# Kernel optimization log

Measured on AMD Instinct MI355X. Metric: run time of the kernel, lower is better.

Reference implementation:

```python
import jax, jax.numpy as jnp
import numpy as np

N, D, K = 8192, 4096, 8
F_HID = D // 4  # 1024


def setup_inputs() -> dict:
    key = jax.random.key(0)
    ks = jax.random.split(key, 8)
    s1 = 1.0 / np.sqrt(2 * D)
    s2 = 1.0 / np.sqrt(F_HID)
    sr = 1.0 / np.sqrt(D)
    return {
        "h_anchor": jax.random.normal(ks[0], (N, D), jnp.float32),
        "h_mask": jax.random.normal(ks[1], (N, D), jnp.float32),
        "Wr": jax.random.normal(ks[2], (K, D), jnp.float32) * sr,
        "br": jnp.zeros((K,), jnp.float32),
        "W1": jax.random.normal(ks[3], (K, F_HID, 2 * D), jnp.float32) * s1,
        "b1": jnp.zeros((K, F_HID), jnp.float32),
        "W2": jax.random.normal(ks[4], (K, D, F_HID), jnp.float32) * s2,
        "b2": jnp.zeros((K, D), jnp.float32),
    }


def reference(h_anchor, h_mask, Wr, br, W1, b1, W2, b2):
    # routing weights: softmax(h_mask @ Wr^T + br) -> [N, K]
    weights = jax.nn.softmax(h_mask @ Wr.T + br, axis=-1)
    # conditioned input: [N, 2D]
    conditioned = jnp.concatenate([h_anchor, h_mask], axis=-1)
    # all-expert first GEMM: [K, N, F]
    h1 = jnp.einsum("nc,kfc->knf", conditioned, W1) + b1[:, None, :]
    h1 = jax.nn.gelu(h1, approximate=False)  # torch nn.GELU default = exact erf
    # second GEMM: [K, N, D]
    expert_out = jnp.einsum("knf,kdf->knd", h1, W2) + b2[:, None, :]
    # softmax-weighted combine over experts -> [N, D]
    return jnp.einsum("knd,nk->nd", expert_out, weights)
```

## Files before the change

### kernel.cpp

```cpp
#include <hip/hip_runtime.h>
#include <hip/hip_bf16.h>
#include <math.h>

typedef __bf16 bf16_t;
typedef __bf16 bf16x8 __attribute__((ext_vector_type(8)));
typedef float  f32x4  __attribute__((ext_vector_type(4)));

#define AS1 __attribute__((address_space(1)))
#define AS3 __attribute__((address_space(3)))

__device__ __forceinline__ void gload_lds16(const bf16_t* g, char* l) {
  __builtin_amdgcn_global_load_lds((const AS1 void*)g, (AS3 void*)l, 16, 0, 0);
}

static constexpr int N_ROWS = 8192;
static constexpr int DDIM   = 4096;
static constexpr int KEXP   = 8;
static constexpr int FHID   = 1024;
static constexpr int KD     = 8192;

__global__ __launch_bounds__(256)
void routing_kernel(const float* __restrict__ hm, const float* __restrict__ Wr,
                    const float* __restrict__ br, float* __restrict__ wgt) {
  const int n = blockIdx.x;
  const int t = threadIdx.x;
  const int wid = t >> 6;
  const float4* row = (const float4*)(hm + (size_t)n * DDIM);
  float4 x[4];
#pragma unroll
  for (int j = 0; j < 4; ++j) x[j] = row[t + j * 256];
  __shared__ float red[KEXP][4];
  float part[KEXP];
#pragma unroll
  for (int k = 0; k < KEXP; ++k) {
    const float4* wr = (const float4*)(Wr + (size_t)k * DDIM);
    float s = 0.f;
#pragma unroll
    for (int j = 0; j < 4; ++j) {
      float4 w4 = wr[t + j * 256];
      s += x[j].x * w4.x + x[j].y * w4.y + x[j].z * w4.z + x[j].w * w4.w;
    }
#pragma unroll
    for (int off = 32; off > 0; off >>= 1) s += __shfl_down(s, off);
    part[k] = s;
  }
  if ((t & 63) == 0) {
#pragma unroll
    for (int k = 0; k < KEXP; ++k) red[k][wid] = part[k];
  }
  __syncthreads();
  if (t == 0) {
    float lg[KEXP];
    float mx = -1e30f;
#pragma unroll
    for (int k = 0; k < KEXP; ++k) {
      lg[k] = red[k][0] + red[k][1] + red[k][2] + red[k][3] + br[k];
      mx = fmaxf(mx, lg[k]);
    }
    float sum = 0.f;
#pragma unroll
    for (int k = 0; k < KEXP; ++k) { lg[k] = expf(lg[k] - mx); sum += lg[k]; }
    float inv = 1.f / sum;
#pragma unroll
    for (int k = 0; k < KEXP; ++k) wgt[(size_t)n * KEXP + k] = lg[k] * inv;
  }
}

__device__ __forceinline__ bf16x8 cvt8(float4 f0, float4 f1) {
  bf16x8 o;
  o[0] = (bf16_t)f0.x; o[1] = (bf16_t)f0.y; o[2] = (bf16_t)f0.z; o[3] = (bf16_t)f0.w;
  o[4] = (bf16_t)f1.x; o[5] = (bf16_t)f1.y; o[6] = (bf16_t)f1.z; o[7] = (bf16_t)f1.w;
  return o;
}

__global__ __launch_bounds__(256)
void conv_cond_kernel(const float* __restrict__ ha, const float* __restrict__ hm,
                      bf16_t* __restrict__ A) {
  size_t c = (size_t)blockIdx.x * 256 + threadIdx.x;
  int n   = (int)(c >> 10);
  int pos = ((int)c & 1023) * 8;
  const float* src = (pos < DDIM) ? ha + (size_t)n * DDIM + pos
                                  : hm + (size_t)n * DDIM + (pos - DDIM);
  float4 f0 = ((const float4*)src)[0];
  float4 f1 = ((const float4*)src)[1];
  *(bf16x8*)(A + c * 8) = cvt8(f0, f1);
}

__global__ __launch_bounds__(256)
void conv_cast_kernel(const float* __restrict__ in, bf16_t* __restrict__ out) {
  size_t c = (size_t)blockIdx.x * 256 + threadIdx.x;
  float4 f0 = ((const float4*)(in + c * 8))[0];
  float4 f1 = ((const float4*)(in + c * 8))[1];
  *(bf16x8*)(out + c * 8) = cvt8(f0, f1);
}

__global__ __launch_bounds__(256)
void conv_w2_kernel(const float* __restrict__ W2, bf16_t* __restrict__ B2) {
  size_t c = (size_t)blockIdx.x * 256 + threadIdx.x;
  int f8 = (int)(c & 127);
  int d  = (int)((c >> 7) & 4095);
  int k  = (int)(c >> 19);
  const float* src = W2 + ((size_t)k * DDIM + d) * FHID + f8 * 8;
  float4 f0 = ((const float4*)src)[0];
  float4 f1 = ((const float4*)src)[1];
  *(bf16x8*)(B2 + (size_t)d * KD + k * FHID + f8 * 8) = cvt8(f0, f1);
}

template <int MODE, int NCOLS>
__global__ __launch_bounds__(512, 2)
void gemm256_kernel(const bf16_t* __restrict__ Amat, const bf16_t* __restrict__ Bmat,
                    void* __restrict__ Cout, const float* __restrict__ bias,
                    const float* __restrict__ wgt) {
  constexpr int BM = 256, BN = 256, BK = 64;
  constexpr int NKT = KD / BK;
  __shared__ char lds_raw[2 * 65536];

  const int tid  = threadIdx.x;
  const int wid  = tid >> 6;
  const int lane = tid & 63;
  const int wr   = wid >> 2;
  const int wc   = wid & 3;

  constexpr int NBN    = NCOLS / BN;
  constexpr int NWIN_N = NBN / 16;
  const int bid = blockIdx.x;
  const int w   = bid >> 8;
  const int sl  = bid & 255;
  const int xcd = sl & 7;
  const int cu  = sl >> 3;
  const int wm  = w / NWIN_N, wn = w % NWIN_N;
  const int bm  = wm * 16 + ((xcd >> 1) << 2) + (cu & 3);
  const int bn  = wn * 16 + ((xcd & 1) << 3) + (cu >> 2);
  const int arow0 = bm * BM;
  const int brow0 = bn * BN;

  const bf16_t* sA[2][2];
  const bf16_t* sB[2][2];
#pragma unroll
  for (int h = 0; h < 2; ++h)
#pragma unroll
    for (int i = 0; i < 2; ++i) {
      int p   = tid * 16 + i * 8192;
      int l   = p ^ (((p >> 7) & 3) << 4) ^ (((p >> 9) & 1) << 6);
      int row = l >> 7, c = l & 127;
      sA[h][i] = Amat + (size_t)(arow0 + h * 128 + row) * KD + (c >> 1);
      sB[h][i] = Bmat + (size_t)(brow0 + h * 128 + row) * KD + (c >> 1);
    }

  const int j = lane >> 4;
  int aoff0[8], boff0[4];
#pragma unroll
  for (int mi = 0; mi < 8; ++mi) {
    int row = wr * 128 + mi * 16 + (lane & 15);
    aoff0[mi] = row * 128 + ((j ^ (row & 3)) << 4) + (((row >> 2) & 1) << 6);
  }
#pragma unroll
  for (int ni = 0; ni < 4; ++ni) {
    int row = wc * 64 + ni * 16 + (lane & 15);
    boff0[ni] = 32768 + row * 128 + ((j ^ (row & 3)) << 4) + (((row >> 2) & 1) << 6);
  }

  f32x4 acc[8][4];
  f32x4 zero = {0.f, 0.f, 0.f, 0.f};
#pragma unroll
  for (int mi = 0; mi < 8; ++mi)
#pragma unroll
    for (int ni = 0; ni < 4; ++ni) acc[mi][ni] = zero;

#define STAGEA(H, TAU)                                                          \
  { const size_t ko = (size_t)((TAU) & (NKT - 1)) * BK;                         \
    char* db = lds_raw + (((TAU) & 1) * 65536) + (H) * 16384 + (wid << 10);     \
    gload_lds16(sA[H][0] + ko, db);                                             \
    gload_lds16(sA[H][1] + ko, db + 8192); }
#define STAGEB(H, TAU)                                                          \
  { const size_t ko = (size_t)((TAU) & (NKT - 1)) * BK;                         \
    char* db = lds_raw + (((TAU) & 1) * 65536) + 32768 + (H) * 16384 + (wid << 10); \
    gload_lds16(sB[H][0] + ko, db);                                             \
    gload_lds16(sB[H][1] + ko, db + 8192); }

  STAGEB(0, 0) STAGEA(0, 0) STAGEA(1, 0) STAGEB(1, 0) STAGEB(0, 1)
  asm volatile("s_waitcnt vmcnt(2)" ::: "memory");
  __builtin_amdgcn_s_barrier();
  __builtin_amdgcn_sched_barrier(0);

  bf16x8 bb[4];

#define SB __builtin_amdgcn_sched_barrier(0);
#define CLUSTER(MI, HH)                                                         \
    _Pragma("unroll")                                                           \
    for (int ni = 0; ni < 4; ++ni)                                              \
      acc[(HH) * 4 + (MI)][ni] = __builtin_amdgcn_mfma_f32_16x16x32_bf16(       \
          aq[MI], bb[ni], acc[(HH) * 4 + (MI)][ni], 0, 0, 0);

#define PHASE(BUFO, HH, SS, STG, GATE)                                          \
  {                                                                             \
    STG;                                                                        \
    SB                                                                          \
    bf16x8 aq[4];                                                               \
    aq[0] = *(const bf16x8*)(lds_raw + (BUFO) + (aoff0[(HH)*4+0] ^ ((SS)*64))); \
    SB                                                                          \
    if ((HH) == 0) {                                                            \
      _Pragma("unroll")                                                         \
      for (int ni = 0; ni < 4; ++ni)                                            \
        bb[ni] = *(const bf16x8*)(lds_raw + (BUFO) + (boff0[ni] ^ ((SS)*64)));  \
      SB                                                                        \
    }                                                                           \
    aq[1] = *(const bf16x8*)(lds_raw + (BUFO) + (aoff0[(HH)*4+1] ^ ((SS)*64))); \
    SB                                                                          \
    aq[2] = *(const bf16x8*)(lds_raw + (BUFO) + (aoff0[(HH)*4+2] ^ ((SS)*64))); \
    SB                                                                          \
    aq[3] = *(const bf16x8*)(lds_raw + (BUFO) + (aoff0[(HH)*4+3] ^ ((SS)*64))); \
    SB                                                                          \
    __builtin_amdgcn_s_setprio(1);                                              \
    asm volatile("s_waitcnt lgkmcnt(3)" ::: "memory");                          \
    SB                                                                          \
    CLUSTER(0, HH)                                                              \
    SB                                                                          \
    asm volatile("s_waitcnt lgkmcnt(2)" ::: "memory");                          \
    SB                                                                          \
    CLUSTER(1, HH)                                                              \
    SB                                                                          \
    asm volatile("s_waitcnt lgkmcnt(1)" ::: "memory");                          \
    SB                                                                          \
    CLUSTER(2, HH)                                                              \
    SB                                                                          \
    asm volatile("s_waitcnt lgkmcnt(0)" ::: "memory");                          \
    SB                                                                          \
    CLUSTER(3, HH)                                                              \
    SB                                                                          \
    __builtin_amdgcn_s_setprio(0);                                              \
    if (GATE) {                                                                 \
      asm volatile("s_waitcnt vmcnt(2)" ::: "memory");                          \
      SB                                                                        \
    }                                                                           \
    __builtin_amdgcn_s_barrier();                                               \
    SB                                                                          \
  }

  for (int t = 0; t < NKT; t += 2) {
    PHASE(0,     0, 0, STAGEA(0, t + 1), 0)
    PHASE(0,     1, 0, STAGEA(1, t + 1), 0)
    PHASE(0,     0, 1, STAGEB(1, t + 1), 0)
    PHASE(0,     1, 1, STAGEB(0, t + 2), 1)
    PHASE(65536, 0, 0, STAGEA(0, t + 2), 0)
    PHASE(65536, 1, 0, STAGEA(1, t + 2), 0)
    PHASE(65536, 0, 1, STAGEB(1, t + 2), 0)
    PHASE(65536, 1, 1, STAGEB(0, t + 3), 1)
  }
#undef PHASE
#undef CLUSTER
#undef SB
#undef STAGEA
#undef STAGEB

  const int grow0 = arow0 + wr * 128 + ((lane >> 4) << 2);
  const int gcol0 = brow0 + wc * 64 + (lane & 15);

  if constexpr (MODE == 1) {
    bf16_t* __restrict__ H = (bf16_t*)Cout;
    const int kexp = brow0 >> 10;
#pragma unroll
    for (int mi = 0; mi < 8; ++mi) {
      float wn4[4];
#pragma unroll
      for (int r = 0; r < 4; ++r)
        wn4[r] = wgt[(size_t)(grow0 + mi * 16 + r) * KEXP + kexp];
#pragma unroll
      for (int ni = 0; ni < 4; ++ni) {
        int col = gcol0 + ni * 16;
        float bv = bias[col];
#pragma unroll
        for (int r = 0; r < 4; ++r) {
          int n = grow0 + mi * 16 + r;
          float x = acc[mi][ni][r] + bv;
          float g = 0.5f * x * (1.f + erff(x * 0.70710678118654752f));
          H[(size_t)n * KD + col] = (bf16_t)(g * wn4[r]);
        }
      }
    }
  } else {
    float* __restrict__ O = (float*)Cout;
    float bcol[4][KEXP];
#pragma unroll
    for (int ni = 0; ni < 4; ++ni)
#pragma unroll
      for (int k = 0; k < KEXP; ++k)
        bcol[ni][k] = bias[(size_t)k * NCOLS + gcol0 + ni * 16];
#pragma unroll
    for (int mi = 0; mi < 8; ++mi)
#pragma unroll
      for (int r = 0; r < 4; ++r) {
        int n = grow0 + mi * 16 + r;
        const float4* wp = (const float4*)(wgt + (size_t)n * KEXP);
        float4 wa = wp[0], wb = wp[1];
        float w8[KEXP] = {wa.x, wa.y, wa.z, wa.w, wb.x, wb.y, wb.z, wb.w};
#pragma unroll
        for (int ni = 0; ni < 4; ++ni) {
          float bb2 = 0.f;
#pragma unroll
          for (int k = 0; k < KEXP; ++k) bb2 += w8[k] * bcol[ni][k];
          O[(size_t)n * NCOLS + gcol0 + ni * 16] = acc[mi][ni][r] + bb2;
        }
      }
  }
}

extern "C" void kernel_launch(void* const* d_in, const int* in_sizes, int n_in,
                              void* d_out, int out_size, void* d_ws, size_t ws_size,
                              hipStream_t stream) {
  const float* h_anchor = (const float*)d_in[0];
  const float* h_mask   = (const float*)d_in[1];
  const float* Wr       = (const float*)d_in[2];
  const float* br       = (const float*)d_in[3];
  const float* W1       = (const float*)d_in[4];
  const float* b1       = (const float*)d_in[5];
  const float* W2       = (const float*)d_in[6];
  const float* b2       = (const float*)d_in[7];
  float* out = (float*)d_out;

  char* ws = (char*)d_ws;
  bf16_t* Abf  = (bf16_t*)(ws);
  bf16_t* W1bf = (bf16_t*)(ws + ((size_t)128 << 20));
  bf16_t* W2bf = (bf16_t*)(ws + ((size_t)256 << 20));
  bf16_t* H1s  = (bf16_t*)(ws + ((size_t)320 << 20));
  float*  wgt  = (float*) (ws + ((size_t)448 << 20));

  routing_kernel<<<N_ROWS, 256, 0, stream>>>(h_mask, Wr, br, wgt);
  conv_cond_kernel<<<(N_ROWS * KD / 8) / 256, 256, 0, stream>>>(h_anchor, h_mask, Abf);
  conv_cast_kernel<<<(KEXP * FHID * 2 * DDIM / 8) / 256, 256, 0, stream>>>(W1, W1bf);
  conv_w2_kernel<<<(KEXP * DDIM * FHID / 8) / 256, 256, 0, stream>>>(W2, W2bf);

  gemm256_kernel<1, 8192><<<(N_ROWS / 256) * (KD / 256), 512, 0, stream>>>(
      Abf, W1bf, (void*)H1s, b1, wgt);
  gemm256_kernel<2, 4096><<<(N_ROWS / 256) * (DDIM / 256), 512, 0, stream>>>(
      H1s, W2bf, (void*)out, b2, wgt);
}
```

Baseline: 1.522 ms.

## Switch GEMM to 32x32x16 MFMA with pre-swizzled LDS layout and simpler pipeline

Rewrites the main GEMM inner loop to use 32x32x16 bf16 MFMA instructions instead of 16x16x32. Operand tiles are staged into LDS in a lane-contiguous layout, so each lane reads its fragment with a plain linear offset and no XOR swizzle. The K-loop now runs one 64-wide k-tile per iteration in four sub-phases, with only two barriers per tile instead of one per phase. The larger MFMA tile is meant to cut LDS reads per FLOP and issue overhead, and the fewer barriers reduce synchronisation cost. The risks are LDS bank conflicts from the new layout and a changed epilogue mapping that must match the 32x32 accumulator layout exactly.

```diff
diff --git a/kernel.cpp b/kernel.cpp
--- a/kernel.cpp
+++ b/kernel.cpp
@@ -5,6 +5,7 @@
 typedef __bf16 bf16_t;
 typedef __bf16 bf16x8 __attribute__((ext_vector_type(8)));
 typedef float  f32x4  __attribute__((ext_vector_type(4)));
+typedef float  f32x16 __attribute__((ext_vector_type(16)));
 
 #define AS1 __attribute__((address_space(1)))
 #define AS3 __attribute__((address_space(3)))
@@ -111,7 +112,7 @@
 void gemm256_kernel(const bf16_t* __restrict__ Amat, const bf16_t* __restrict__ Bmat,
                     void* __restrict__ Cout, const float* __restrict__ bias,
                     const float* __restrict__ wgt) {
-  constexpr int BM = 256, BN = 256, BK = 64;
+  constexpr int BK = 64;
   constexpr int NKT = KD / BK;
   __shared__ char lds_raw[2 * 65536];
 
@@ -121,7 +122,7 @@
   const int wr   = wid >> 2;
   const int wc   = wid & 3;
 
-  constexpr int NBN    = NCOLS / BN;
+  constexpr int NBN    = NCOLS / 256;
   constexpr int NWIN_N = NBN / 16;
   const int bid = blockIdx.x;
   const int w   = bid >> 8;
@@ -131,176 +132,154 @@
   const int wm  = w / NWIN_N, wn = w % NWIN_N;
   const int bm  = wm * 16 + ((xcd >> 1) << 2) + (cu & 3);
   const int bn  = wn * 16 + ((xcd & 1) << 3) + (cu >> 2);
-  const int arow0 = bm * BM;
-  const int brow0 = bn * BN;
-
-  const bf16_t* sA[2][2];
-  const bf16_t* sB[2][2];
-#pragma unroll
-  for (int h = 0; h < 2; ++h)
-#pragma unroll
-    for (int i = 0; i < 2; ++i) {
-      int p   = tid * 16 + i * 8192;
-      int l   = p ^ (((p >> 7) & 3) << 4) ^ (((p >> 9) & 1) << 6);
-      int row = l >> 7, c = l & 127;
-      sA[h][i] = Amat + (size_t)(arow0 + h * 128 + row) * KD + (c >> 1);
-      sB[h][i] = Bmat + (size_t)(brow0 + h * 128 + row) * KD + (c >> 1);
-    }
-
-  const int j = lane >> 4;
-  int aoff0[8], boff0[4];
-#pragma unroll
-  for (int mi = 0; mi < 8; ++mi) {
-    int row = wr * 128 + mi * 16 + (lane & 15);
-    aoff0[mi] = row * 128 + ((j ^ (row & 3)) << 4) + (((row >> 2) & 1) << 6);
-  }
-#pragma unroll
-  for (int ni = 0; ni < 4; ++ni) {
-    int row = wc * 64 + ni * 16 + (lane & 15);
-    boff0[ni] = 32768 + row * 128 + ((j ^ (row & 3)) << 4) + (((row >> 2) & 1) << 6);
-  }
-
-  f32x4 acc[8][4];
-  f32x4 zero = {0.f, 0.f, 0.f, 0.f};
-#pragma unroll
-  for (int mi = 0; mi < 8; ++mi)
-#pragma unroll
-    for (int ni = 0; ni < 4; ++ni) acc[mi][ni] = zero;
-
-#define STAGEA(H, TAU)                                                          \
-  { const size_t ko = (size_t)((TAU) & (NKT - 1)) * BK;                         \
-    char* db = lds_raw + (((TAU) & 1) * 65536) + (H) * 16384 + (wid << 10);     \
-    gload_lds16(sA[H][0] + ko, db);                                             \
-    gload_lds16(sA[H][1] + ko, db + 8192); }
-#define STAGEB(H, TAU)                                                          \
-  { const size_t ko = (size_t)((TAU) & (NKT - 1)) * BK;                         \
-    char* db = lds_raw + (((TAU) & 1) * 65536) + 32768 + (H) * 16384 + (wid << 10); \
-    gload_lds16(sB[H][0] + ko, db);                                             \
-    gload_lds16(sB[H][1] + ko, db + 8192); }
-
-  STAGEB(0, 0) STAGEA(0, 0) STAGEA(1, 0) STAGEB(1, 0) STAGEB(0, 1)
-  asm volatile("s_waitcnt vmcnt(2)" ::: "memory");
+  const int arow0 = bm * 256;
+  const int brow0 = bn * 256;
+
+  const int b0 = 2 * wid, b1 = 2 * wid + 1;
+  const int dA0 = ((b0 >> 2) & 1) * 16384 + (b0 >> 3) * 4096 + (b0 & 3) * 1024;
+  const int dA1 = ((b1 >> 2) & 1) * 16384 + (b1 >> 3) * 4096 + (b1 & 3) * 1024;
+  const int dB0 = 32768 + (b0 >> 3) * 8192 + (b0 & 7) * 1024;
+  const int dB1 = 32768 + (b1 >> 3) * 8192 + (b1 & 7) * 1024;
+  const bf16_t* srcA0 = Amat + (size_t)(arow0 + ((b0 >> 2) & 1) * 128 + (b0 & 3) * 32 + (lane & 31)) * KD
+                        + (b0 >> 3) * 16 + (lane >> 5) * 8;
+  const bf16_t* srcA1 = Amat + (size_t)(arow0 + ((b1 >> 2) & 1) * 128 + (b1 & 3) * 32 + (lane & 31)) * KD
+                        + (b1 >> 3) * 16 + (lane >> 5) * 8;
+  const bf16_t* srcB0 = Bmat + (size_t)(brow0 + (b0 & 7) * 32 + (lane & 31)) * KD
+                        + (b0 >> 3) * 16 + (lane >> 5) * 8;
+  const bf16_t* srcB1 = Bmat + (size_t)(brow0 + (b1 & 7) * 32 + (lane & 31)) * KD
+                        + (b1 >> 3) * 16 + (lane >> 5) * 8;
+
+  f32x16 acc[4][2];
+#pragma unroll
+  for (int mi = 0; mi < 4; ++mi)
+#pragma unroll
+    for (int nj = 0; nj < 2; ++nj)
+#pragma unroll
+      for (int r = 0; r < 16; ++r) acc[mi][nj][r] = 0.f;
+
+  gload_lds16(srcA0, lds_raw + dA0);
+  gload_lds16(srcA1, lds_raw + dA1);
+  gload_lds16(srcB0, lds_raw + dB0);
+  gload_lds16(srcB1, lds_raw + dB1);
+  gload_lds16(srcA0 + 32, lds_raw + dA0 + 8192);
+  gload_lds16(srcA1 + 32, lds_raw + dA1 + 8192);
+  gload_lds16(srcB0 + 32, lds_raw + dB0 + 16384);
+  gload_lds16(srcB1 + 32, lds_raw + dB1 + 16384);
+  asm volatile("s_waitcnt vmcnt(0)" ::: "memory");
   __builtin_amdgcn_s_barrier();
   __builtin_amdgcn_sched_barrier(0);
 
-  bf16x8 bb[4];
-
 #define SB __builtin_amdgcn_sched_barrier(0);
-#define CLUSTER(MI, HH)                                                         \
-    _Pragma("unroll")                                                           \
-    for (int ni = 0; ni < 4; ++ni)                                              \
-      acc[(HH) * 4 + (MI)][ni] = __builtin_amdgcn_mfma_f32_16x16x32_bf16(       \
-          aq[MI], bb[ni], acc[(HH) * 4 + (MI)][ni], 0, 0, 0);
-
-#define PHASE(BUFO, HH, SS, STG, GATE)                                          \
+#define MM(MI)                                                                  \
+    acc[MI][0] = __builtin_amdgcn_mfma_f32_32x32x16_bf16(aq[MI], qb0,           \
+                                                         acc[MI][0], 0, 0, 0);  \
+    acc[MI][1] = __builtin_amdgcn_mfma_f32_32x32x16_bf16(aq[MI], qb1,           \
+                                                         acc[MI][1], 0, 0, 0);
+
+#define PH(SS, STG0, STG1, GATE)                                                \
   {                                                                             \
-    STG;                                                                        \
+    STG0;                                                                       \
+    STG1;                                                                       \
+    SB                                                                          \
+    bf16x8 qb0 = *(const bf16x8*)(bB + (SS) * 8192);                            \
+    bf16x8 qb1 = *(const bf16x8*)(bB + (SS) * 8192 + 1024);                     \
     SB                                                                          \
     bf16x8 aq[4];                                                               \
-    aq[0] = *(const bf16x8*)(lds_raw + (BUFO) + (aoff0[(HH)*4+0] ^ ((SS)*64))); \
-    SB                                                                          \
-    if ((HH) == 0) {                                                            \
-      _Pragma("unroll")                                                         \
-      for (int ni = 0; ni < 4; ++ni)                                            \
-        bb[ni] = *(const bf16x8*)(lds_raw + (BUFO) + (boff0[ni] ^ ((SS)*64)));  \
+    aq[0] = *(const bf16x8*)(bA + (SS) * 4096);                                 \
+    SB                                                                          \
+    aq[1] = *(const bf16x8*)(bA + (SS) * 4096 + 1024);                          \
+    SB                                                                          \
+    aq[2] = *(const bf16x8*)(bA + (SS) * 4096 + 2048);                          \
+    SB                                                                          \
+    aq[3] = *(const bf16x8*)(bA + (SS) * 4096 + 3072);                          \
+    SB                                                                          \
+    __builtin_amdgcn_s_setprio(1);                                              \
+    asm volatile("s_waitcnt lgkmcnt(3)" ::: "memory");                          \
+    SB                                                                          \
+    MM(0)                                                                       \
+    SB                                                                          \
+    asm volatile("s_waitcnt lgkmcnt(2)" ::: "memory");                          \
+    SB                                                                          \
+    MM(1)                                                                       \
+    SB                                                                          \
+    asm volatile("s_waitcnt lgkmcnt(1)" ::: "memory");                          \
+    SB                                                                          \
+    MM(2)                                                                       \
+    SB                                                                          \
+    asm volatile("s_waitcnt lgkmcnt(0)" ::: "memory");                          \
+    SB                                                                          \
+    MM(3)                                                                       \
+    SB                                                                          \
+    __builtin_amdgcn_s_setprio(0);                                              \
+    if (GATE) {                                                                 \
+      asm volatile("s_waitcnt vmcnt(4)" ::: "memory");                          \
+      SB                                                                        \
+      __builtin_amdgcn_s_barrier();                                             \
       SB                                                                        \
     }                                                                           \
-    aq[1] = *(const bf16x8*)(lds_raw + (BUFO) + (aoff0[(HH)*4+1] ^ ((SS)*64))); \
-    SB                                                                          \
-    aq[2] = *(const bf16x8*)(lds_raw + (BUFO) + (aoff0[(HH)*4+2] ^ ((SS)*64))); \
-    SB                                                                          \
-    aq[3] = *(const bf16x8*)(lds_raw + (BUFO) + (aoff0[(HH)*4+3] ^ ((SS)*64))); \
-    SB                                                                          \
-    __builtin_amdgcn_s_setprio(1);                                              \
-    asm volatile("s_waitcnt lgkmcnt(3)" ::: "memory");                          \
-    SB                                                                          \
-    CLUSTER(0, HH)                                                              \
-    SB                                                                          \
-    asm volatile("s_waitcnt lgkmcnt(2)" ::: "memory");                          \
-    SB                                                                          \
-    CLUSTER(1, HH)                                                              \
-    SB                                                                          \
-    asm volatile("s_waitcnt lgkmcnt(1)" ::: "memory");                          \
-    SB                                                                          \
-    CLUSTER(2, HH)                                                              \
-    SB                                                                          \
-    asm volatile("s_waitcnt lgkmcnt(0)" ::: "memory");                          \
-    SB                                                                          \
-    CLUSTER(3, HH)                                                              \
-    SB                                                                          \
-    __builtin_amdgcn_s_setprio(0);                                              \
-    if (GATE) {                                                                 \
-      asm volatile("s_waitcnt vmcnt(2)" ::: "memory");                          \
-      SB                                                                        \
-    }                                                                           \
-    __builtin_amdgcn_s_barrier();                                               \
-    SB                                                                          \
-  }
-
-  for (int t = 0; t < NKT; t += 2) {
-    PHASE(0,     0, 0, STAGEA(0, t + 1), 0)
-    PHASE(0,     1, 0, STAGEA(1, t + 1), 0)
-    PHASE(0,     0, 1, STAGEB(1, t + 1), 0)
-    PHASE(0,     1, 1, STAGEB(0, t + 2), 1)
-    PHASE(65536, 0, 0, STAGEA(0, t + 2), 0)
-    PHASE(65536, 1, 0, STAGEA(1, t + 2), 0)
-    PHASE(65536, 0, 1, STAGEB(1, t + 2), 0)
-    PHASE(65536, 1, 1, STAGEB(0, t + 3), 1)
-  }
-#undef PHASE
-#undef CLUSTER
+  }
+
+  int cur = 0;
+  for (int t = 0; t < NKT; ++t) {
+    const size_t ko = (size_t)((t + 1) & (NKT - 1)) * BK;
+    char* nb = lds_raw + (cur ^ 65536);
+    const char* bA = lds_raw + cur + wr * 16384 + lane * 16;
+    const char* bB = lds_raw + cur + 32768 + wc * 2048 + lane * 16;
+    PH(0, gload_lds16(srcA0 + ko, nb + dA0),
+          gload_lds16(srcA1 + ko, nb + dA1), 0)
+    PH(1, gload_lds16(srcB0 + ko, nb + dB0),
+          gload_lds16(srcB1 + ko, nb + dB1), 1)
+    PH(2, gload_lds16(srcA0 + ko + 32, nb + dA0 + 8192),
+          gload_lds16(srcA1 + ko + 32, nb + dA1 + 8192), 0)
+    PH(3, gload_lds16(srcB0 + ko + 32, nb + dB0 + 16384),
+          gload_lds16(srcB1 + ko + 32, nb + dB1 + 16384), 1)
+    cur ^= 65536;
+  }
+#undef PH
+#undef MM
 #undef SB
-#undef STAGEA
-#undef STAGEB
-
-  const int grow0 = arow0 + wr * 128 + ((lane >> 4) << 2);
-  const int gcol0 = brow0 + wc * 64 + (lane & 15);
+
+  const int rbase = arow0 + wr * 128 + ((lane >> 5) << 2);
+  const int cbase = brow0 + wc * 64 + (lane & 31);
 
   if constexpr (MODE == 1) {
     bf16_t* __restrict__ H = (bf16_t*)Cout;
     const int kexp = brow0 >> 10;
-#pragma unroll
-    for (int mi = 0; mi < 8; ++mi) {
-      float wn4[4];
-#pragma unroll
-      for (int r = 0; r < 4; ++r)
-        wn4[r] = wgt[(size_t)(grow0 + mi * 16 + r) * KEXP + kexp];
-#pragma unroll
-      for (int ni = 0; ni < 4; ++ni) {
-        int col = gcol0 + ni * 16;
-        float bv = bias[col];
-#pragma unroll
-        for (int r = 0; r < 4; ++r) {
-          int n = grow0 + mi * 16 + r;
-          float x = acc[mi][ni][r] + bv;
+    float bv[2] = {bias[cbase], bias[cbase + 32]};
+#pragma unroll
+    for (int mi = 0; mi < 4; ++mi)
+#pragma unroll
+      for (int r = 0; r < 16; ++r) {
+        int n = rbase + mi * 32 + (r & 3) + 8 * (r >> 2);
+        float wn4 = wgt[(size_t)n * KEXP + kexp];
+#pragma unroll
+        for (int nj = 0; nj < 2; ++nj) {
+          float x = acc[mi][nj][r] + bv[nj];
           float g = 0.5f * x * (1.f + erff(x * 0.70710678118654752f));
-          H[(size_t)n * KD + col] = (bf16_t)(g * wn4[r]);
+          H[(size_t)n * KD + cbase + nj * 32] = (bf16_t)(g * wn4);
         }
       }
-    }
   } else {
     float* __restrict__ O = (float*)Cout;
-    float bcol[4][KEXP];
-#pragma unroll
-    for (int ni = 0; ni < 4; ++ni)
-#pragma unroll
-      for (int k = 0; k < KEXP; ++k)
-        bcol[ni][k] = bias[(size_t)k * NCOLS + gcol0 + ni * 16];
-#pragma unroll
-    for (int mi = 0; mi < 8; ++mi)
-#pragma unroll
-      for (int r = 0; r < 4; ++r) {
-        int n = grow0 + mi * 16 + r;
+    float bc0[KEXP], bc1[KEXP];
+#pragma unroll
+    for (int k = 0; k < KEXP; ++k) {
+      bc0[k] = bias[(size_t)k * NCOLS + cbase];
+      bc1[k] = bias[(size_t)k * NCOLS + cbase + 32];
+    }
+#pragma unroll
+    for (int mi = 0; mi < 4; ++mi)
+#pragma unroll
+      for (int r = 0; r < 16; ++r) {
+        int n = rbase + mi * 32 + (r & 3) + 8 * (r >> 2);
         const float4* wp = (const float4*)(wgt + (size_t)n * KEXP);
         float4 wa = wp[0], wb = wp[1];
         float w8[KEXP] = {wa.x, wa.y, wa.z, wa.w, wb.x, wb.y, wb.z, wb.w};
-#pragma unroll
-        for (int ni = 0; ni < 4; ++ni) {
-          float bb2 = 0.f;
-#pragma unroll
-          for (int k = 0; k < KEXP; ++k) bb2 += w8[k] * bcol[ni][k];
-          O[(size_t)n * NCOLS + gcol0 + ni * 16] = acc[mi][ni][r] + bb2;
-        }
+        float s0 = 0.f, s1 = 0.f;
+#pragma unroll
+        for (int k = 0; k < KEXP; ++k) { s0 += w8[k] * bc0[k]; s1 += w8[k] * bc1[k]; }
+        O[(size_t)n * NCOLS + cbase]      = acc[mi][0][r] + s0;
+        O[(size_t)n * NCOLS + cbase + 32] = acc[mi][1][r] + s1;
       }
   }
 }
```

Result: slower. 2.132 ms (+40.1%).
